# Performance work log

Measured on AMD Instinct MI355X. Metric: run time of the kernel, lower is better.

Reference implementation:

```python
import jax, jax.numpy as jnp
import numpy as np

CONTEXT = 3  # config['context']
B, H, W = 8, 256, 256
NBR = 2 * CONTEXT  # number of similarity branches


def _conv(x, w, b):
    # x: [N, Cin, H, W], w: [Cout, Cin, kh, kw], SAME padding, stride 1
    y = jax.lax.conv_general_dilated(x, w, (1, 1), 'SAME',
                                     dimension_numbers=('NCHW', 'OIHW', 'NCHW'))
    return y + b[None, :, None, None]


def setup_inputs() -> dict:
    key = jax.random.key(0)
    ks = jax.random.split(key, 5)
    x = jax.random.normal(ks[0], (B, 2 * CONTEXT + 1, H, W), dtype=jnp.float32)
    # kaiming-ish scaled inits
    W1 = jax.random.normal(ks[1], (NBR, 64, 2, 3, 3), dtype=jnp.float32) * (2.0 / (64 * 9)) ** 0.5
    b1 = jnp.zeros((NBR, 64), dtype=jnp.float32)
    W2 = jax.random.normal(ks[2], (NBR, 1, 64, 1, 1), dtype=jnp.float32) * (2.0 / 1) ** 0.5 * 0.1
    b2 = jnp.zeros((NBR, 1), dtype=jnp.float32)
    Wm = jax.random.normal(ks[3], (7, 7, 3, 3), dtype=jnp.float32) * (2.0 / (7 * 9)) ** 0.5
    bm = jnp.zeros((7,), dtype=jnp.float32)
    return {'x': x, 'W1': W1, 'b1': b1, 'W2': W2, 'b2': b2, 'Wm': Wm, 'bm': bm}


def reference(x, W1, b1, W2, b2, Wm, bm):
    # mode == 'context' path just returns x; this implements the main path.
    base = x[:, CONTEXT:CONTEXT + 1]                                  # [B,1,H,W]
    checks = jnp.concatenate([x[:, :CONTEXT], x[:, CONTEXT + 1:]], axis=1)  # [B,6,H,W]
    check_e = checks[:, :, None]                                      # [B,6,1,H,W]
    base_e = jnp.broadcast_to(base[:, None], check_e.shape)           # [B,6,1,H,W]
    # channel order: pre-frames -> (base, check); post-frames -> (check, base)
    ch0 = jnp.concatenate([base_e[:, :CONTEXT], check_e[:, CONTEXT:]], axis=2 - 2 + 2)  # placeholder
    ch0 = jnp.concatenate([base_e[:, :CONTEXT], check_e[:, CONTEXT:]], axis=1)
    ch1 = jnp.concatenate([check_e[:, :CONTEXT], base_e[:, CONTEXT:]], axis=1)
    pairs = jnp.concatenate([ch0, ch1], axis=2)                       # [B,6,2,H,W]
    pairs = jnp.swapaxes(pairs, 0, 1)                                 # [6,B,2,H,W]

    def branch(pair, w1, bb1, w2, bb2):
        h = jax.nn.relu(_conv(pair, w1, bb1))                         # [B,64,H,W]
        return jax.nn.sigmoid(_conv(h, w2, bb2))                      # [B,1,H,W]

    sims = jax.vmap(branch)(pairs, W1, b1, W2, b2)                    # [6,B,1,H,W]
    weighted = sims[:, :, 0] * jnp.swapaxes(checks, 0, 1)             # [6,B,H,W]
    weighted = jnp.swapaxes(weighted, 0, 1)                           # [B,6,H,W]
    combined = jnp.concatenate([weighted[:, :CONTEXT], base, weighted[:, CONTEXT:]], axis=1)  # [B,7,H,W]
    return _conv(combined, Wm, bm)                                    # [B,7,H,W]
```

## Files before the change

kernel.cpp:

```cpp
#include <hip/hip_runtime.h>
#include <math.h>

#define Bn 8
#define Hn 256
#define Wn 256
#define HW (Hn * Wn)
#define ROWS 8
#define RP 264
#define ZW (20 * RP)

typedef __attribute__((ext_vector_type(8))) short bf16x8;
typedef __attribute__((ext_vector_type(4))) float f32x4;
typedef __attribute__((ext_vector_type(2))) float f32x2;

__device__ __forceinline__ unsigned int pk_bits(unsigned int lo,
                                                unsigned int hi) {
  return __builtin_amdgcn_perm(hi, lo, 0x07060302u);
}
__device__ __forceinline__ unsigned int pk_bf16(float lo, float hi) {
  return pk_bits(__float_as_uint(lo), __float_as_uint(hi));
}

__device__ __constant__ const int T0c[8] = {0, 1, 2, 9, 10, 11, 3, 4};
__device__ __constant__ const int T1c[8] = {6, 7, 8, 15, 16, 17, 12, 13};
__device__ __constant__ const int T2c[8] = {5, 14, -1, -1, -1, -1, -1, -1};

__global__ __launch_bounds__(256, 4) void sim_kernel(
    const float* __restrict__ x,
    const float* __restrict__ W1,
    const float* __restrict__ b1,
    const float* __restrict__ W2,
    const float* __restrict__ b2,
    float* __restrict__ comb)
{
  __shared__ float rowsF[20 * RP + 64];
  __shared__ uint4 wq[4][64];

  int bi = blockIdx.x;
  int n  = bi >> 8;
  int b  = (bi >> 5) & 7;
  int h0 = (bi & 31) * ROWS;
  int cc = (n < 3) ? n : n + 1;
  int t = threadIdx.x;

  const float* xb     = x + (size_t)b * 7 * HW;
  const float* basep  = xb + 3 * HW;
  const float* checkp = xb + (size_t)cc * HW;

  {
    int f = t >> 6, qq = (t >> 4) & 3, m = t & 15;
    int bsrc = (n < 3) ? 0 : 1;
    const float* wch = W1 + ((size_t)(n * 64 + 16 * f + m)) * 18;
    unsigned int kv[4];
#pragma unroll
    for (int jj = 0; jj < 4; ++jj) {
      int ja = 2 * jj, jb = 2 * jj + 1;
      int ta = (qq == 0) ? T0c[ja] : (qq == 1) ? T1c[ja]
               : (qq == 2) ? T2c[ja] : -1;
      int tb = (qq == 0) ? T0c[jb] : (qq == 1) ? T1c[jb]
               : (qq == 2) ? T2c[jb] : -1;
      float va = 0.f, vb = 0.f;
      if (ta >= 0) {
        int pl = ta / 9, rem = ta - pl * 9;
        va = wch[(pl ? 1 - bsrc : bsrc) * 9 + rem];
      }
      if (tb >= 0) {
        int pl = tb / 9, rem = tb - pl * 9;
        vb = wch[(pl ? 1 - bsrc : bsrc) * 9 + rem];
      }
      kv[jj] = pk_bf16(va, vb);
    }
    wq[f][(qq << 4) + m] = make_uint4(kv[0], kv[1], kv[2], kv[3]);
  }

  int lane = t & 63, wvid = t >> 6;
  int q = lane >> 4, m_ = lane & 15;
  f32x2 w2A[4], w2B[4];
  f32x4 b1vv[4];
#pragma unroll
  for (int f = 0; f < 4; ++f) {
    float4 tw = *(const float4*)&W2[n * 64 + 16 * f + 4 * q];
    float4 tb = *(const float4*)&b1[n * 64 + 16 * f + 4 * q];
    w2A[f][0] = tw.x; w2A[f][1] = tw.y;
    w2B[f][0] = tw.z; w2B[f][1] = tw.w;
    b1vv[f][0] = tb.x; b1vv[f][1] = tb.y;
    b1vv[f][2] = tb.z; b1vv[f][3] = tb.w;
  }
  float bb = b2[n];

  {
    int col = (t & 63) << 2;
#pragma unroll
    for (int it = 0; it < 5; ++it) {
      int rf = it * 4 + (t >> 6);
      int pl = (rf >= 10) ? 1 : 0;
      int j  = rf - pl * 10;
      int hh = h0 - 1 + j;
      const float* src = pl ? checkp : basep;
      float4 val = make_float4(0.f, 0.f, 0.f, 0.f);
      if ((unsigned)hh < (unsigned)Hn)
        val = *(const float4*)(src + hh * Wn + col);
      *(float4*)&rowsF[rf * RP + 4 + col] = val;
    }
    if (t < 20) {
      rowsF[t * RP + 3] = 0.f;
      rowsF[t * RP + 260] = 0.f;
    }
    if (t >= 192) rowsF[ZW + (t - 192)] = 0.f;
  }

  const unsigned int* rowsU = (const unsigned int*)rowsF;
  unsigned int addr[8];
#pragma unroll
  for (int jh = 0; jh < 8; ++jh) {
    int tap = (q == 0) ? T0c[jh] : (q == 1) ? T1c[jh]
              : (q == 2) ? T2c[jh] : -1;
    if (tap >= 0) {
      int pl = tap / 9, rem = tap - pl * 9;
      int rr = rem / 3, dx = rem - rr * 3;
      addr[jh] = (pl * 10 + rr) * RP + 3 + dx + wvid * 64 + m_;
    } else {
      addr[jh] = (unsigned)ZW;
    }
  }
  unsigned int stepA = (q <= 2) ? (unsigned)RP : 0u;
  unsigned int stepB = (q < 2) ? (unsigned)RP : 0u;
  int bpaddr = ((lane ^ 32) << 2);

  __syncthreads();

  bf16x8 afrag[4];
#pragma unroll
  for (int f = 0; f < 4; ++f) afrag[f] = *(const bf16x8*)&wq[f][lane];

  float* combcc = comb + ((size_t)b * 7 + cc) * HW;
  int pxs = wvid * 64 + lane;

  auto compute2 = [&](const unsigned int* dbuf, float& gA, float& gB) {
    union { unsigned int u[4]; bf16x8 v; } p0, p1;
#pragma unroll
    for (int jj = 0; jj < 4; ++jj) {
      p0.u[jj] = pk_bits(dbuf[2 * jj], dbuf[2 * jj + 1]);
      p1.u[jj] = pk_bits(dbuf[8 + 2 * jj], dbuf[8 + 2 * jj + 1]);
    }
    f32x4 acc0[4], acc1[4];
#pragma unroll
    for (int f = 0; f < 4; ++f) {
      acc0[f] = __builtin_amdgcn_mfma_f32_16x16x32_bf16(afrag[f], p0.v,
                                                        b1vv[f], 0, 0, 0);
      acc1[f] = __builtin_amdgcn_mfma_f32_16x16x32_bf16(afrag[f], p1.v,
                                                        b1vv[f], 0, 0, 0);
    }
    f32x2 sA0 = {0.f, 0.f}, sB0 = {0.f, 0.f};
    f32x2 sA1 = {0.f, 0.f}, sB1 = {0.f, 0.f};
#pragma unroll
    for (int f = 0; f < 4; ++f) {
      f32x2 a01, a23, c01, c23;
      a01[0] = acc0[f][0]; a01[1] = acc0[f][1];
      a23[0] = acc0[f][2]; a23[1] = acc0[f][3];
      c01[0] = acc1[f][0]; c01[1] = acc1[f][1];
      c23[0] = acc1[f][2]; c23[1] = acc1[f][3];
      a01 = __builtin_elementwise_max(a01, (f32x2)0.f);
      a23 = __builtin_elementwise_max(a23, (f32x2)0.f);
      c01 = __builtin_elementwise_max(c01, (f32x2)0.f);
      c23 = __builtin_elementwise_max(c23, (f32x2)0.f);
      sA0 += w2A[f] * a01;
      sB0 += w2B[f] * a23;
      sA1 += w2A[f] * c01;
      sB1 += w2B[f] * c23;
    }
    float sp0 = (sA0[0] + sB0[0]) + (sA0[1] + sB0[1]);
    float sp1 = (sA1[0] + sB1[0]) + (sA1[1] + sB1[1]);
    sp0 += __int_as_float(
        __builtin_amdgcn_ds_swizzle(__float_as_int(sp0), 0x401F));
    sp1 += __int_as_float(
        __builtin_amdgcn_ds_swizzle(__float_as_int(sp1), 0x401F));
    sp0 += __int_as_float(
        __builtin_amdgcn_ds_bpermute(bpaddr, __float_as_int(sp0)));
    sp1 += __int_as_float(
        __builtin_amdgcn_ds_bpermute(bpaddr, __float_as_int(sp1)));
    sp0 += bb;
    sp1 += bb;
    float e0 = __builtin_amdgcn_exp2f(sp0 * -1.442695041f);
    float e1 = __builtin_amdgcn_exp2f(sp1 * -1.442695041f);
    gA = __builtin_amdgcn_rcpf(1.f + e0);
    gB = __builtin_amdgcn_rcpf(1.f + e1);
  };

  unsigned int bufA[16], bufB[16];
#pragma unroll
  for (int jh = 0; jh < 8; ++jh) {
    bufA[jh]     = rowsU[addr[jh]];
    bufA[jh + 8] = rowsU[addr[jh] + 16];
  }

#pragma unroll 1
  for (int r = 0; r < ROWS; ++r) {
    float ccv = rowsF[(10 + r + 1) * RP + 4 + pxs];

#pragma unroll
    for (int jh = 0; jh < 8; ++jh) {
      bufB[jh]     = rowsU[addr[jh] + 32];
      bufB[jh + 8] = rowsU[addr[jh] + 48];
    }

    float g0, g1, g2, g3;
    compute2(bufA, g0, g1);

    if (r < ROWS - 1) {
#pragma unroll
      for (int jh = 0; jh < 8; ++jh) {
        addr[jh] += (jh < 2) ? stepA : stepB;
        bufA[jh]     = rowsU[addr[jh]];
        bufA[jh + 8] = rowsU[addr[jh] + 16];
      }
    }

    compute2(bufB, g2, g3);

    int hi = lane >> 4;
    float gsel = (hi == 0) ? g0 : (hi == 1) ? g1 : (hi == 2) ? g2 : g3;
    combcc[(h0 + r) * Wn + pxs] = gsel * ccv;
  }
}

__global__ __launch_bounds__(512) void mix_kernel(
    const float* __restrict__ comb,
    const float* __restrict__ x,
    const float* __restrict__ Wm,
    const float* __restrict__ bm,
    float* __restrict__ out)
{
  __shared__ float mr[42 * RP];

  int bi = blockIdx.x;
  int b  = bi >> 6;
  int h0 = (bi & 63) << 2;
  int t = threadIdx.x;

  for (int u = t; u < 42 * 64; u += 512) {
    int rf = u >> 6;
    int col = (u & 63) << 2;
    int ic = rf / 6, j = rf - ic * 6;
    int hh = h0 - 1 + j;
    const float* src = (ic == 3) ? (x + ((size_t)b * 7 + 3) * HW)
                                 : (comb + ((size_t)b * 7 + ic) * HW);
    float4 v = make_float4(0.f, 0.f, 0.f, 0.f);
    if ((unsigned)hh < (unsigned)Hn)
      v = *(const float4*)(src + hh * Wn + col);
    *(float4*)&mr[rf * RP + 4 + col] = v;
  }
  if (t < 42) {
    mr[t * RP + 3] = 0.f;
    mr[t * RP + 260] = 0.f;
  }
  __syncthreads();

  int r   = t >> 7;
  int px0 = (t & 127) << 1;
  int h   = h0 + r;

  float acc[7][2];
#pragma unroll
  for (int oc = 0; oc < 7; ++oc) {
    float bv = bm[oc];
    acc[oc][0] = bv;
    acc[oc][1] = bv;
  }

#pragma unroll 1
  for (int ic = 0; ic < 7; ++ic) {
    float w[3][4];
#pragma unroll
    for (int dy = 0; dy < 3; ++dy) {
      const float* rp = &mr[(ic * 6 + r + dy) * RP + 3 + px0];
      w[dy][0] = rp[0]; w[dy][1] = rp[1];
      w[dy][2] = rp[2]; w[dy][3] = rp[3];
    }
    const float* wp = Wm + ic * 9;
#pragma unroll
    for (int oc = 0; oc < 7; ++oc) {
      const float* wo = wp + oc * 63;
#pragma unroll
      for (int dy = 0; dy < 3; ++dy)
#pragma unroll
        for (int dx = 0; dx < 3; ++dx) {
          float wvv = wo[dy * 3 + dx];
          acc[oc][0] = fmaf(wvv, w[dy][0 + dx], acc[oc][0]);
          acc[oc][1] = fmaf(wvv, w[dy][1 + dx], acc[oc][1]);
        }
    }
  }

  float* ob = out + (size_t)b * 7 * HW + h * Wn + px0;
#pragma unroll
  for (int oc = 0; oc < 7; ++oc)
    *(float2*)(ob + (size_t)oc * HW) = make_float2(acc[oc][0], acc[oc][1]);
}

extern "C" void kernel_launch(void* const* d_in, const int* in_sizes, int n_in,
                              void* d_out, int out_size, void* d_ws, size_t ws_size,
                              hipStream_t stream) {
  const float* x  = (const float*)d_in[0];
  const float* W1 = (const float*)d_in[1];
  const float* b1 = (const float*)d_in[2];
  const float* W2 = (const float*)d_in[3];
  const float* b2 = (const float*)d_in[4];
  const float* Wm = (const float*)d_in[5];
  const float* bm = (const float*)d_in[6];
  float* out  = (float*)d_out;
  float* comb = (float*)d_ws;

  sim_kernel<<<6 * 8 * (Hn / ROWS), 256, 0, stream>>>(x, W1, b1, W2, b2, comb);
  mix_kernel<<<8 * (Hn / 4), 512, 0, stream>>>(comb, x, Wm, bm, out);
}
```

Baseline: 116.5 us.

## Fuse similarity branches and mix conv into one kernel with halo recompute

Merges the similarity kernel and the 3x3 mix convolution into a single kernel. Each block loads all 7 input planes for 4 output rows plus halo, computes each branch's weighted similarity map for 6 rows in shared memory, and accumulates the mix convolution in registers. This drops the global round trip of the intermediate combined tensor and one launch. In exchange it recomputes the similarity on halo rows (6 rows per 4 outputs), serializes the six branches within a block with extra barriers, and uses more shared memory, which lowers occupancy.

```diff
diff --git a/kernel.cpp b/kernel.cpp
--- a/kernel.cpp
+++ b/kernel.cpp
@@ -5,9 +5,14 @@
 #define Hn 256
 #define Wn 256
 #define HW (Hn * Wn)
-#define ROWS 8
+#define R 4
+#define XR 8
 #define RP 264
-#define ZW (20 * RP)
+#define PSZ (XR * RP)
+#define ZWOFF 14800
+#define CBOFF 14864
+#define WQOFF 16448
+#define STOT  17472
 
 typedef __attribute__((ext_vector_type(8))) short bf16x8;
 typedef __attribute__((ext_vector_type(4))) float f32x4;
@@ -25,92 +30,56 @@
 __device__ __constant__ const int T1c[8] = {6, 7, 8, 15, 16, 17, 12, 13};
 __device__ __constant__ const int T2c[8] = {5, 14, -1, -1, -1, -1, -1, -1};
 
-__global__ __launch_bounds__(256, 4) void sim_kernel(
+__global__ __launch_bounds__(256, 2) void fused_kernel(
     const float* __restrict__ x,
     const float* __restrict__ W1,
     const float* __restrict__ b1,
     const float* __restrict__ W2,
     const float* __restrict__ b2,
-    float* __restrict__ comb)
+    const float* __restrict__ Wm,
+    const float* __restrict__ bm,
+    float* __restrict__ out)
 {
-  __shared__ float rowsF[20 * RP + 64];
-  __shared__ uint4 wq[4][64];
+  __shared__ float S[STOT];
 
   int bi = blockIdx.x;
-  int n  = bi >> 8;
-  int b  = (bi >> 5) & 7;
-  int h0 = (bi & 31) * ROWS;
-  int cc = (n < 3) ? n : n + 1;
-  int t = threadIdx.x;
-
-  const float* xb     = x + (size_t)b * 7 * HW;
-  const float* basep  = xb + 3 * HW;
-  const float* checkp = xb + (size_t)cc * HW;
-
-  {
-    int f = t >> 6, qq = (t >> 4) & 3, m = t & 15;
-    int bsrc = (n < 3) ? 0 : 1;
-    const float* wch = W1 + ((size_t)(n * 64 + 16 * f + m)) * 18;
-    unsigned int kv[4];
-#pragma unroll
-    for (int jj = 0; jj < 4; ++jj) {
-      int ja = 2 * jj, jb = 2 * jj + 1;
-      int ta = (qq == 0) ? T0c[ja] : (qq == 1) ? T1c[ja]
-               : (qq == 2) ? T2c[ja] : -1;
-      int tb = (qq == 0) ? T0c[jb] : (qq == 1) ? T1c[jb]
-               : (qq == 2) ? T2c[jb] : -1;
-      float va = 0.f, vb = 0.f;
-      if (ta >= 0) {
-        int pl = ta / 9, rem = ta - pl * 9;
-        va = wch[(pl ? 1 - bsrc : bsrc) * 9 + rem];
-      }
-      if (tb >= 0) {
-        int pl = tb / 9, rem = tb - pl * 9;
-        vb = wch[(pl ? 1 - bsrc : bsrc) * 9 + rem];
-      }
-      kv[jj] = pk_bf16(va, vb);
-    }
-    wq[f][(qq << 4) + m] = make_uint4(kv[0], kv[1], kv[2], kv[3]);
-  }
+  int b  = bi >> 6;
+  int h0 = (bi & 63) << 2;
+  int t  = threadIdx.x;
+
+  const unsigned int* rowsU = (const unsigned int*)S;
+  uint4* wq = (uint4*)&S[WQOFF];
+
+  for (int u = t; u < 56 * 64; u += 256) {
+    int rf = u >> 6;
+    int p  = rf >> 3, j = rf & 7;
+    int col = (u & 63) << 2;
+    int po = p * PSZ + (p ? 16 : 0);
+    int sp = (p == 0) ? 3 : ((p <= 3) ? p - 1 : p);
+    int hh = h0 - 2 + j;
+    float4 v = make_float4(0.f, 0.f, 0.f, 0.f);
+    if ((unsigned)hh < (unsigned)Hn)
+      v = *(const float4*)(x + ((size_t)b * 7 + sp) * HW + hh * Wn + col);
+    *(float4*)&S[po + j * RP + 4 + col] = v;
+  }
+  if (t < 56) {
+    int p = t >> 3, j = t & 7;
+    int po = p * PSZ + (p ? 16 : 0);
+    S[po + j * RP + 3] = 0.f;
+    S[po + j * RP + 260] = 0.f;
+  }
+  if (t < 6) {
+    S[CBOFF + t * RP + 3] = 0.f;
+    S[CBOFF + t * RP + 260] = 0.f;
+  }
+  if (t >= 192) S[ZWOFF + (t - 192)] = 0.f;
 
   int lane = t & 63, wvid = t >> 6;
   int q = lane >> 4, m_ = lane & 15;
-  f32x2 w2A[4], w2B[4];
-  f32x4 b1vv[4];
-#pragma unroll
-  for (int f = 0; f < 4; ++f) {
-    float4 tw = *(const float4*)&W2[n * 64 + 16 * f + 4 * q];
-    float4 tb = *(const float4*)&b1[n * 64 + 16 * f + 4 * q];
-    w2A[f][0] = tw.x; w2A[f][1] = tw.y;
-    w2B[f][0] = tw.z; w2B[f][1] = tw.w;
-    b1vv[f][0] = tb.x; b1vv[f][1] = tb.y;
-    b1vv[f][2] = tb.z; b1vv[f][3] = tb.w;
-  }
-  float bb = b2[n];
-
-  {
-    int col = (t & 63) << 2;
-#pragma unroll
-    for (int it = 0; it < 5; ++it) {
-      int rf = it * 4 + (t >> 6);
-      int pl = (rf >= 10) ? 1 : 0;
-      int j  = rf - pl * 10;
-      int hh = h0 - 1 + j;
-      const float* src = pl ? checkp : basep;
-      float4 val = make_float4(0.f, 0.f, 0.f, 0.f);
-      if ((unsigned)hh < (unsigned)Hn)
-        val = *(const float4*)(src + hh * Wn + col);
-      *(float4*)&rowsF[rf * RP + 4 + col] = val;
-    }
-    if (t < 20) {
-      rowsF[t * RP + 3] = 0.f;
-      rowsF[t * RP + 260] = 0.f;
-    }
-    if (t >= 192) rowsF[ZW + (t - 192)] = 0.f;
-  }
-
-  const unsigned int* rowsU = (const unsigned int*)rowsF;
-  unsigned int addr[8];
+  int pxs = wvid * 64 + lane;
+  int bpaddr = ((lane ^ 32) << 2);
+
+  unsigned int rowterm[8], plbits = 0;
 #pragma unroll
   for (int jh = 0; jh < 8; ++jh) {
     int tap = (q == 0) ? T0c[jh] : (q == 1) ? T1c[jh]
@@ -118,184 +87,224 @@
     if (tap >= 0) {
       int pl = tap / 9, rem = tap - pl * 9;
       int rr = rem / 3, dx = rem - rr * 3;
-      addr[jh] = (pl * 10 + rr) * RP + 3 + dx + wvid * 64 + m_;
+      if (pl) plbits |= 1u << jh;
+      rowterm[jh] = rr * RP + 3 + dx + wvid * 64 + m_;
     } else {
-      addr[jh] = (unsigned)ZW;
+      rowterm[jh] = 0u;
     }
   }
   unsigned int stepA = (q <= 2) ? (unsigned)RP : 0u;
   unsigned int stepB = (q < 2) ? (unsigned)RP : 0u;
-  int bpaddr = ((lane ^ 32) << 2);
+
+  int r0  = t >> 7;
+  int pxm = (t & 127) << 1;
+
+  float acc[7][2][2];
+#pragma unroll
+  for (int oc = 0; oc < 7; ++oc) {
+    float bv = bm[oc];
+    acc[oc][0][0] = bv; acc[oc][0][1] = bv;
+    acc[oc][1][0] = bv; acc[oc][1][1] = bv;
+  }
 
   __syncthreads();
 
-  bf16x8 afrag[4];
-#pragma unroll
-  for (int f = 0; f < 4; ++f) afrag[f] = *(const bf16x8*)&wq[f][lane];
-
-  float* combcc = comb + ((size_t)b * 7 + cc) * HW;
-  int pxs = wvid * 64 + lane;
-
-  auto compute2 = [&](const unsigned int* dbuf, float& gA, float& gB) {
-    union { unsigned int u[4]; bf16x8 v; } p0, p1;
-#pragma unroll
-    for (int jj = 0; jj < 4; ++jj) {
-      p0.u[jj] = pk_bits(dbuf[2 * jj], dbuf[2 * jj + 1]);
-      p1.u[jj] = pk_bits(dbuf[8 + 2 * jj], dbuf[8 + 2 * jj + 1]);
-    }
-    f32x4 acc0[4], acc1[4];
+  {
+    float v[5][4];
+#pragma unroll
+    for (int k2 = 0; k2 < 5; ++k2) {
+      const float* rp = &S[(r0 + k2 + 1) * RP + 3 + pxm];
+      v[k2][0] = rp[0]; v[k2][1] = rp[1]; v[k2][2] = rp[2]; v[k2][3] = rp[3];
+    }
+#pragma unroll
+    for (int oc = 0; oc < 7; ++oc) {
+      const float* wo = Wm + oc * 63 + 3 * 9;
+#pragma unroll
+      for (int dy = 0; dy < 3; ++dy) {
+        float w0 = wo[dy * 3], w1 = wo[dy * 3 + 1], w2 = wo[dy * 3 + 2];
+#pragma unroll
+        for (int rs = 0; rs < 2; ++rs) {
+          float* vv = v[rs * 2 + dy];
+          acc[oc][rs][0] = fmaf(w0, vv[0],
+                            fmaf(w1, vv[1], fmaf(w2, vv[2], acc[oc][rs][0])));
+          acc[oc][rs][1] = fmaf(w0, vv[1],
+                            fmaf(w1, vv[2], fmaf(w2, vv[3], acc[oc][rs][1])));
+        }
+      }
+    }
+  }
+
+#pragma unroll 1
+  for (int n = 0; n < 6; ++n) {
+    int cc = (n < 3) ? n : n + 1;
+    int poff = (1 + n) * PSZ + 16;
+
+    {
+      int f = t >> 6, qq = (t >> 4) & 3, m = t & 15;
+      int bsrc = (n < 3) ? 0 : 1;
+      const float* wch = W1 + ((size_t)(n * 64 + 16 * f + m)) * 18;
+      unsigned int kv[4];
+#pragma unroll
+      for (int jj = 0; jj < 4; ++jj) {
+        int ja = 2 * jj, jb = 2 * jj + 1;
+        int ta = (qq == 0) ? T0c[ja] : (qq == 1) ? T1c[ja]
+                 : (qq == 2) ? T2c[ja] : -1;
+        int tb = (qq == 0) ? T0c[jb] : (qq == 1) ? T1c[jb]
+                 : (qq == 2) ? T2c[jb] : -1;
+        float va = 0.f, vb = 0.f;
+        if (ta >= 0) {
+          int pl = ta / 9, rem = ta - pl * 9;
+          va = wch[(pl ? 1 - bsrc : bsrc) * 9 + rem];
+        }
+        if (tb >= 0) {
+          int pl = tb / 9, rem = tb - pl * 9;
+          vb = wch[(pl ? 1 - bsrc : bsrc) * 9 + rem];
+        }
+        kv[jj] = pk_bf16(va, vb);
+      }
+      wq[f * 64 + (qq << 4) + m] = make_uint4(kv[0], kv[1], kv[2], kv[3]);
+    }
+
+    f32x2 w2A[4], w2B[4];
+    f32x4 b1vv[4];
 #pragma unroll
     for (int f = 0; f < 4; ++f) {
-      acc0[f] = __builtin_amdgcn_mfma_f32_16x16x32_bf16(afrag[f], p0.v,
-                                                        b1vv[f], 0, 0, 0);
-      acc1[f] = __builtin_amdgcn_mfma_f32_16x16x32_bf16(afrag[f], p1.v,
-                                                        b1vv[f], 0, 0, 0);
-    }
-    f32x2 sA0 = {0.f, 0.f}, sB0 = {0.f, 0.f};
-    f32x2 sA1 = {0.f, 0.f}, sB1 = {0.f, 0.f};
-#pragma unroll
-    for (int f = 0; f < 4; ++f) {
-      f32x2 a01, a23, c01, c23;
-      a01[0] = acc0[f][0]; a01[1] = acc0[f][1];
-      a23[0] = acc0[f][2]; a23[1] = acc0[f][3];
-      c01[0] = acc1[f][0]; c01[1] = acc1[f][1];
-      c23[0] = acc1[f][2]; c23[1] = acc1[f][3];
-      a01 = __builtin_elementwise_max(a01, (f32x2)0.f);
-      a23 = __builtin_elementwise_max(a23, (f32x2)0.f);
-      c01 = __builtin_elementwise_max(c01, (f32x2)0.f);
-      c23 = __builtin_elementwise_max(c23, (f32x2)0.f);
-      sA0 += w2A[f] * a01;
-      sB0 += w2B[f] * a23;
-      sA1 += w2A[f] * c01;
-      sB1 += w2B[f] * c23;
-    }
-    float sp0 = (sA0[0] + sB0[0]) + (sA0[1] + sB0[1]);
-    float sp1 = (sA1[0] + sB1[0]) + (sA1[1] + sB1[1]);
-    sp0 += __int_as_float(
-        __builtin_amdgcn_ds_swizzle(__float_as_int(sp0), 0x401F));
-    sp1 += __int_as_float(
-        __builtin_amdgcn_ds_swizzle(__float_as_int(sp1), 0x401F));
-    sp0 += __int_as_float(
-        __builtin_amdgcn_ds_bpermute(bpaddr, __float_as_int(sp0)));
-    sp1 += __int_as_float(
-        __builtin_amdgcn_ds_bpermute(bpaddr, __float_as_int(sp1)));
-    sp0 += bb;
-    sp1 += bb;
-    float e0 = __builtin_amdgcn_exp2f(sp0 * -1.442695041f);
-    float e1 = __builtin_amdgcn_exp2f(sp1 * -1.442695041f);
-    gA = __builtin_amdgcn_rcpf(1.f + e0);
-    gB = __builtin_amdgcn_rcpf(1.f + e1);
-  };
-
-  unsigned int bufA[16], bufB[16];
-#pragma unroll
-  for (int jh = 0; jh < 8; ++jh) {
-    bufA[jh]     = rowsU[addr[jh]];
-    bufA[jh + 8] = rowsU[addr[jh] + 16];
-  }
+      float4 tw = *(const float4*)&W2[n * 64 + 16 * f + 4 * q];
+      float4 tb = *(const float4*)&b1[n * 64 + 16 * f + 4 * q];
+      w2A[f][0] = tw.x; w2A[f][1] = tw.y;
+      w2B[f][0] = tw.z; w2B[f][1] = tw.w;
+      b1vv[f][0] = tb.x; b1vv[f][1] = tb.y;
+      b1vv[f][2] = tb.z; b1vv[f][3] = tb.w;
+    }
+    float bb = b2[n];
+
+    unsigned int addr[8];
+#pragma unroll
+    for (int jh = 0; jh < 8; ++jh) {
+      bool live = (jh < 2) ? (q <= 2) : (q < 2);
+      addr[jh] = live
+          ? rowterm[jh] + (((plbits >> jh) & 1u) ? (unsigned)poff : 0u)
+          : (unsigned)ZWOFF;
+    }
+
+    __syncthreads();
+
+    bf16x8 afrag[4];
+#pragma unroll
+    for (int f = 0; f < 4; ++f) afrag[f] = *(const bf16x8*)&wq[f * 64 + lane];
+
+    auto compute2 = [&](const unsigned int* dbuf, float& gA, float& gB) {
+      union { unsigned int u[4]; bf16x8 v; } p0, p1;
+#pragma unroll
+      for (int jj = 0; jj < 4; ++jj) {
+        p0.u[jj] = pk_bits(dbuf[2 * jj], dbuf[2 * jj + 1]);
+        p1.u[jj] = pk_bits(dbuf[8 + 2 * jj], dbuf[8 + 2 * jj + 1]);
+      }
+      f32x4 acc0[4], acc1[4];
+#pragma unroll
+      for (int f = 0; f < 4; ++f) {
+        acc0[f] = __builtin_amdgcn_mfma_f32_16x16x32_bf16(afrag[f], p0.v,
+                                                          b1vv[f], 0, 0, 0);
+        acc1[f] = __builtin_amdgcn_mfma_f32_16x16x32_bf16(afrag[f], p1.v,
+                                                          b1vv[f], 0, 0, 0);
+      }
+      f32x2 sA0 = {0.f, 0.f}, sB0 = {0.f, 0.f};
+      f32x2 sA1 = {0.f, 0.f}, sB1 = {0.f, 0.f};
+#pragma unroll
+      for (int f = 0; f < 4; ++f) {
+        f32x2 a01, a23, c01, c23;
+        a01[0] = acc0[f][0]; a01[1] = acc0[f][1];
+        a23[0] = acc0[f][2]; a23[1] = acc0[f][3];
+        c01[0] = acc1[f][0]; c01[1] = acc1[f][1];
+        c23[0] = acc1[f][2]; c23[1] = acc1[f][3];
+        a01 = __builtin_elementwise_max(a01, (f32x2)0.f);
+        a23 = __builtin_elementwise_max(a23, (f32x2)0.f);
+        c01 = __builtin_elementwise_max(c01, (f32x2)0.f);
+        c23 = __builtin_elementwise_max(c23, (f32x2)0.f);
+        sA0 += w2A[f] * a01;
+        sB0 += w2B[f] * a23;
+        sA1 += w2A[f] * c01;
+        sB1 += w2B[f] * c23;
+      }
+      float sp0 = (sA0[0] + sB0[0]) + (sA0[1] + sB0[1]);
+      float sp1 = (sA1[0] + sB1[0]) + (sA1[1] + sB1[1]);
+      sp0 += __int_as_float(
+          __builtin_amdgcn_ds_swizzle(__float_as_int(sp0), 0x401F));
+      sp1 += __int_as_float(
+          __builtin_amdgcn_ds_swizzle(__float_as_int(sp1), 0x401F));
+      sp0 += __int_as_float(
+          __builtin_amdgcn_ds_bpermute(bpaddr, __float_as_int(sp0)));
+      sp1 += __int_as_float(
+          __builtin_amdgcn_ds_bpermute(bpaddr, __float_as_int(sp1)));
+      sp0 += bb;
+      sp1 += bb;
+      float e0 = __builtin_amdgcn_exp2f(sp0 * -1.442695041f);
+      float e1 = __builtin_amdgcn_exp2f(sp1 * -1.442695041f);
+      gA = __builtin_amdgcn_rcpf(1.f + e0);
+      gB = __builtin_amdgcn_rcpf(1.f + e1);
+    };
 
 #pragma unroll 1
-  for (int r = 0; r < ROWS; ++r) {
-    float ccv = rowsF[(10 + r + 1) * RP + 4 + pxs];
-
-#pragma unroll
-    for (int jh = 0; jh < 8; ++jh) {
-      bufB[jh]     = rowsU[addr[jh] + 32];
-      bufB[jh + 8] = rowsU[addr[jh] + 48];
-    }
-
-    float g0, g1, g2, g3;
-    compute2(bufA, g0, g1);
-
-    if (r < ROWS - 1) {
+    for (int k = 0; k < 6; ++k) {
+      unsigned int bufA[16], bufB[16];
 #pragma unroll
       for (int jh = 0; jh < 8; ++jh) {
-        addr[jh] += (jh < 2) ? stepA : stepB;
         bufA[jh]     = rowsU[addr[jh]];
         bufA[jh + 8] = rowsU[addr[jh] + 16];
-      }
-    }
-
-    compute2(bufB, g2, g3);
-
-    int hi = lane >> 4;
-    float gsel = (hi == 0) ? g0 : (hi == 1) ? g1 : (hi == 2) ? g2 : g3;
-    combcc[(h0 + r) * Wn + pxs] = gsel * ccv;
-  }
-}
-
-__global__ __launch_bounds__(512) void mix_kernel(
-    const float* __restrict__ comb,
-    const float* __restrict__ x,
-    const float* __restrict__ Wm,
-    const float* __restrict__ bm,
-    float* __restrict__ out)
-{
-  __shared__ float mr[42 * RP];
-
-  int bi = blockIdx.x;
-  int b  = bi >> 6;
-  int h0 = (bi & 63) << 2;
-  int t = threadIdx.x;
-
-  for (int u = t; u < 42 * 64; u += 512) {
-    int rf = u >> 6;
-    int col = (u & 63) << 2;
-    int ic = rf / 6, j = rf - ic * 6;
-    int hh = h0 - 1 + j;
-    const float* src = (ic == 3) ? (x + ((size_t)b * 7 + 3) * HW)
-                                 : (comb + ((size_t)b * 7 + ic) * HW);
-    float4 v = make_float4(0.f, 0.f, 0.f, 0.f);
-    if ((unsigned)hh < (unsigned)Hn)
-      v = *(const float4*)(src + hh * Wn + col);
-    *(float4*)&mr[rf * RP + 4 + col] = v;
-  }
-  if (t < 42) {
-    mr[t * RP + 3] = 0.f;
-    mr[t * RP + 260] = 0.f;
-  }
-  __syncthreads();
-
-  int r   = t >> 7;
-  int px0 = (t & 127) << 1;
-  int h   = h0 + r;
-
-  float acc[7][2];
+        bufB[jh]     = rowsU[addr[jh] + 32];
+        bufB[jh + 8] = rowsU[addr[jh] + 48];
+      }
+      float g0, g1, g2, g3;
+      compute2(bufA, g0, g1);
+      compute2(bufB, g2, g3);
+
+      int hi = lane >> 4;
+      float gsel = (hi == 0) ? g0 : (hi == 1) ? g1 : (hi == 2) ? g2 : g3;
+      float ccv = S[poff + (k + 1) * RP + 4 + pxs];
+      S[CBOFF + k * RP + 4 + pxs] = gsel * ccv;
+
+#pragma unroll
+      for (int jh = 0; jh < 8; ++jh) addr[jh] += (jh < 2) ? stepA : stepB;
+    }
+
+    __syncthreads();
+
+    {
+      float v[5][4];
+#pragma unroll
+      for (int k2 = 0; k2 < 5; ++k2) {
+        const float* rp = &S[CBOFF + (r0 + k2) * RP + 3 + pxm];
+        v[k2][0] = rp[0]; v[k2][1] = rp[1]; v[k2][2] = rp[2]; v[k2][3] = rp[3];
+      }
+#pragma unroll
+      for (int oc = 0; oc < 7; ++oc) {
+        const float* wo = Wm + oc * 63 + cc * 9;
+#pragma unroll
+        for (int dy = 0; dy < 3; ++dy) {
+          float w0 = wo[dy * 3], w1 = wo[dy * 3 + 1], w2 = wo[dy * 3 + 2];
+#pragma unroll
+          for (int rs = 0; rs < 2; ++rs) {
+            float* vv = v[rs * 2 + dy];
+            acc[oc][rs][0] = fmaf(w0, vv[0],
+                              fmaf(w1, vv[1], fmaf(w2, vv[2], acc[oc][rs][0])));
+            acc[oc][rs][1] = fmaf(w0, vv[1],
+                              fmaf(w1, vv[2], fmaf(w2, vv[3], acc[oc][rs][1])));
+          }
+        }
+      }
+    }
+  }
+
+  float* ob = out + (size_t)b * 7 * HW;
 #pragma unroll
   for (int oc = 0; oc < 7; ++oc) {
-    float bv = bm[oc];
-    acc[oc][0] = bv;
-    acc[oc][1] = bv;
-  }
-
-#pragma unroll 1
-  for (int ic = 0; ic < 7; ++ic) {
-    float w[3][4];
-#pragma unroll
-    for (int dy = 0; dy < 3; ++dy) {
-      const float* rp = &mr[(ic * 6 + r + dy) * RP + 3 + px0];
-      w[dy][0] = rp[0]; w[dy][1] = rp[1];
-      w[dy][2] = rp[2]; w[dy][3] = rp[3];
-    }
-    const float* wp = Wm + ic * 9;
-#pragma unroll
-    for (int oc = 0; oc < 7; ++oc) {
-      const float* wo = wp + oc * 63;
-#pragma unroll
-      for (int dy = 0; dy < 3; ++dy)
-#pragma unroll
-        for (int dx = 0; dx < 3; ++dx) {
-          float wvv = wo[dy * 3 + dx];
-          acc[oc][0] = fmaf(wvv, w[dy][0 + dx], acc[oc][0]);
-          acc[oc][1] = fmaf(wvv, w[dy][1 + dx], acc[oc][1]);
-        }
-    }
-  }
-
-  float* ob = out + (size_t)b * 7 * HW + h * Wn + px0;
-#pragma unroll
-  for (int oc = 0; oc < 7; ++oc)
-    *(float2*)(ob + (size_t)oc * HW) = make_float2(acc[oc][0], acc[oc][1]);
+#pragma unroll
+    for (int rs = 0; rs < 2; ++rs) {
+      int h = h0 + r0 + 2 * rs;
+      *(float2*)(ob + (size_t)oc * HW + h * Wn + pxm) =
+          make_float2(acc[oc][rs][0], acc[oc][rs][1]);
+    }
+  }
 }
 
 extern "C" void kernel_launch(void* const* d_in, const int* in_sizes, int n_in,
@@ -308,9 +317,8 @@
   const float* b2 = (const float*)d_in[4];
   const float* Wm = (const float*)d_in[5];
   const float* bm = (const float*)d_in[6];
-  float* out  = (float*)d_out;
-  float* comb = (float*)d_ws;
-
-  sim_kernel<<<6 * 8 * (Hn / ROWS), 256, 0, stream>>>(x, W1, b1, W2, b2, comb);
-  mix_kernel<<<8 * (Hn / 4), 512, 0, stream>>>(comb, x, Wm, bm, out);
+  float* out = (float*)d_out;
+
+  fused_kernel<<<8 * (Hn / R), 256, 0, stream>>>(x, W1, b1, W2, b2, Wm, bm,
+                                                 out);
 }
```

Result: slower. 133.5 us (+14.6%).
